# Kernel tuning notes

Hardware: AMD Instinct MI355X
Metric: run time of the kernel (lower is better)

## Reference

```python
import jax, jax.numpy as jnp
import numpy as np

EMBED_DIM = 1024
NUM_HEAD = 16
HEAD_DIM = EMBED_DIM // NUM_HEAD


def _linear_params(key, in_dim, out_dim):
    kw, kb = jax.random.split(key)
    bound = 1.0 / np.sqrt(in_dim)
    W = jax.random.uniform(kw, (out_dim, in_dim), minval=-bound, maxval=bound, dtype=jnp.float32)
    b = jax.random.uniform(kb, (out_dim,), minval=-bound, maxval=bound, dtype=jnp.float32)
    return W, b


def setup_inputs() -> dict:
    key = jax.random.key(0)
    ks = jax.random.split(key, 7)
    N, S, E = 2, 2048, EMBED_DIM
    k = jax.random.normal(ks[0], (N, S, E), dtype=jnp.float32)
    q = jax.random.normal(ks[1], (N, S, E), dtype=jnp.float32)
    v = jax.random.normal(ks[2], (N, S, E), dtype=jnp.float32)
    Wk, bk = _linear_params(ks[3], E, E)
    Wq, bq = _linear_params(ks[4], E, E)
    Wv, bv = _linear_params(ks[5], E, E)
    Wo, bo = _linear_params(ks[6], E, E)
    return {"key": k, "query": q, "value": v,
            "Wk": Wk, "bk": bk, "Wq": Wq, "bq": bq,
            "Wv": Wv, "bv": bv, "Wo": Wo, "bo": bo}


def reference(key, query, value, Wk, bk, Wq, bq, Wv, bv, Wo, bo):
    N, S_in, E = key.shape
    S_out = query.shape[1]
    H, D = NUM_HEAD, HEAD_DIM
    # projections (torch Linear: x @ W.T + b), split heads -> [N, H, S, D]
    k = (key @ Wk.T + bk).reshape(N, S_in, H, D).transpose(0, 2, 1, 3)
    q = (query @ Wq.T + bq).reshape(N, S_out, H, D).transpose(0, 2, 1, 3)
    v = (value @ Wv.T + bv).reshape(N, S_in, H, D).transpose(0, 2, 1, 3)
    # unfused attention: full [N,H,S_out,S_in] score matrix, scale, softmax
    weight = jnp.einsum("nhqd,nhkd->nhqk", q, k) / jnp.sqrt(jnp.float32(D))
    weight = jax.nn.softmax(weight, axis=-1)
    attn = jnp.einsum("nhqk,nhkd->nhqd", weight, v)  # [N,H,S_out,D]
    attn = attn.transpose(0, 2, 1, 3).reshape(N, S_out, E)
    return attn @ Wo.T + bo
```

## Files before the change

### kernel.cpp

```cpp
#include <hip/hip_runtime.h>

constexpr int E  = 1024;
constexpr int NH = 16;
constexpr int HD = 64;
constexpr int S  = 2048;
constexpr int NB = 2;
constexpr int M  = NB * S;

typedef unsigned short u16;
typedef _Float16 f16;
typedef __attribute__((ext_vector_type(8))) _Float16 h8v;
typedef __attribute__((ext_vector_type(2))) __fp16 hp2v;
typedef __attribute__((ext_vector_type(4))) float f4v;

__device__ __forceinline__ f4v mfmaH(h8v a, h8v b, f4v c) {
    return __builtin_amdgcn_mfma_f32_16x16x32_f16(a, b, c, 0, 0, 0);
}
__device__ __forceinline__ u16 f16bits(float x) {
    union { f16 h; u16 u; } t; t.h = (f16)x; return t.u;
}
__device__ __forceinline__ unsigned pkrtz(float a, float b) {
    union { hp2v h; unsigned u; } t;
    t.h = __builtin_amdgcn_cvt_pkrtz(a, b);
    return t.u;
}
__device__ __forceinline__ float fexp2(float x) {
    float r;
    asm("v_exp_f32 %0, %1" : "=v"(r) : "v"(x));
    return r;
}
typedef const __attribute__((address_space(1))) void gvoid;
typedef __attribute__((address_space(3))) void lvoid;
__device__ __forceinline__ void load_lds16(const u16* g, u16* l) {
    __builtin_amdgcn_global_load_lds((gvoid*)g, (lvoid*)l, 16, 0, 0);
}

__global__ __launch_bounds__(256)
void cvt_f16(const float* __restrict__ q, const float* __restrict__ k,
             const float* __restrict__ v,
             const float* __restrict__ wq, const float* __restrict__ wk,
             const float* __restrict__ wv, const float* __restrict__ wo,
             u16* __restrict__ out)
{
    const size_t ME = (size_t)M * E, EE = (size_t)E * E;
    const int z = blockIdx.y;
    const float* src = (z == 0) ? q : (z == 1) ? k : (z == 2) ? v
                     : (z == 3) ? wq : (z == 4) ? wk : (z == 5) ? wv : wo;
    const size_t len = (z < 3) ? ME : EE;
    u16* dst = out + ((z < 3) ? (size_t)z * ME : 3 * ME + (size_t)(z - 3) * EE);
    for (size_t i = ((size_t)blockIdx.x * 256 + threadIdx.x) * 8; i < len;
         i += (size_t)gridDim.x * 256 * 8) {
        float4 a = *reinterpret_cast<const float4*>(src + i);
        float4 b = *reinterpret_cast<const float4*>(src + i + 4);
        h8v o;
        o[0] = (f16)a.x; o[1] = (f16)a.y; o[2] = (f16)a.z; o[3] = (f16)a.w;
        o[4] = (f16)b.x; o[5] = (f16)b.y; o[6] = (f16)b.z; o[7] = (f16)b.w;
        *reinterpret_cast<h8v*>(dst + i) = o;
    }
}

__device__ __forceinline__ void gemm16_core(const u16* __restrict__ A,
                                            const u16* __restrict__ W,
                                            int bm, int bn, u16* lds, f4v acc[4][4])
{
    const int tid  = threadIdx.x;
    const int lane = tid & 63;
    const int wid  = tid >> 6;
    const int g = lane >> 4, c = lane & 15;
    const int wr = wid >> 1, wc = wid & 1;
    const int lrow = lane >> 3;
    const int lslot = lane & 7;
    const int sslot = lslot ^ lrow;

    for (int k0 = 0; k0 < E; k0 += 64) {
        #pragma unroll
        for (int i = 0; i < 4; ++i) {
            int rbase = wid * 32 + i * 8;
            load_lds16(A + (size_t)(bm + rbase + lrow) * E + k0 + (sslot << 3),
                       &lds[rbase * 64]);
            load_lds16(W + (size_t)(bn + rbase + lrow) * E + k0 + (sslot << 3),
                       &lds[8192 + rbase * 64]);
        }
        __syncthreads();

        h8v a[4][2];
        #pragma unroll
        for (int mf = 0; mf < 4; ++mf) {
            int row = wr * 64 + mf * 16 + c;
            #pragma unroll
            for (int ks = 0; ks < 2; ++ks)
                a[mf][ks] = *reinterpret_cast<h8v*>(
                    &lds[row * 64 + ((((ks << 2) | g) ^ (c & 7)) << 3)]);
        }
        #pragma unroll
        for (int nf = 0; nf < 4; ++nf) {
            int row = wc * 64 + nf * 16 + c;
            #pragma unroll
            for (int ks = 0; ks < 2; ++ks) {
                h8v b = *reinterpret_cast<h8v*>(
                    &lds[8192 + row * 64 + ((((ks << 2) | g) ^ (c & 7)) << 3)]);
                #pragma unroll
                for (int mf = 0; mf < 4; ++mf)
                    acc[mf][nf] = mfmaH(a[mf][ks], b, acc[mf][nf]);
            }
        }
        __syncthreads();
    }
}

__global__ __launch_bounds__(256, 3)
void qkv_gemm(const u16* __restrict__ qf, const u16* __restrict__ kf,
              const u16* __restrict__ vf,
              const u16* __restrict__ wqf, const u16* __restrict__ wkf,
              const u16* __restrict__ wvf,
              const float* __restrict__ bq, const float* __restrict__ bk,
              const float* __restrict__ bv,
              u16* __restrict__ Qattn, u16* __restrict__ KV, float scaleQ)
{
    __shared__ __align__(16) u16 lds[16384];
    const int z = blockIdx.z;
    const u16* A = (z == 0) ? qf : (z == 1) ? kf : vf;
    const u16* W = (z == 0) ? wqf : (z == 1) ? wkf : wvf;
    const float* bias = (z == 0) ? bq : (z == 1) ? bk : bv;
    const float scl = (z == 0) ? scaleQ : 1.0f;
    const int bm = blockIdx.x * 128, bn = blockIdx.y * 128;

    f4v acc[4][4];
    #pragma unroll
    for (int a = 0; a < 4; ++a)
        #pragma unroll
        for (int b = 0; b < 4; ++b) acc[a][b] = (f4v){0.f, 0.f, 0.f, 0.f};

    gemm16_core(A, W, bm, bn, lds, acc);

    const int lane = threadIdx.x & 63;
    const int g = lane >> 4, c = lane & 15;
    const int wid = threadIdx.x >> 6;
    const int wr = wid >> 1, wc = wid & 1;
    float bcol[4];
    #pragma unroll
    for (int nf = 0; nf < 4; ++nf) bcol[nf] = bias[bn + wc * 64 + nf * 16 + c];

    #pragma unroll
    for (int mf = 0; mf < 4; ++mf)
        #pragma unroll
        for (int r = 0; r < 4; ++r) {
            int m  = bm + wr * 64 + mf * 16 + g * 4 + r;
            int nb = m >> 11, sp = m & (S - 1);
            #pragma unroll
            for (int nf = 0; nf < 4; ++nf) {
                int ncol = bn + wc * 64 + nf * 16 + c;
                int h = ncol >> 6, d = ncol & 63;
                int bh_ = nb * NH + h;
                u16 hb = f16bits((acc[mf][nf][r] + bcol[nf]) * scl);
                if (z == 0) {
                    Qattn[((size_t)bh_ * S + sp) * HD + d] = hb;
                } else if (z == 1) {
                    int t = sp >> 6, kk = (sp >> 4) & 3, cc = sp & 15;
                    int ds = d >> 5, gg = (d >> 3) & 3, j = d & 7;
                    KV[((size_t)bh_ * 32 + t) * 8192 +
                       ((size_t)((kk * 2 + ds) * 64 + gg * 16 + cc)) * 8 + j] = hb;
                } else {
                    int t = sp >> 6, rem = sp & 63;
                    int s2 = rem >> 5, bb = (rem >> 4) & 1, gg = (rem >> 2) & 3, a2 = rem & 3;
                    int j = 4 * bb + a2;
                    int df = d >> 4, cc = d & 15;
                    KV[((size_t)bh_ * 32 + t) * 8192 + 4096 +
                       ((size_t)((df * 2 + s2) * 64 + gg * 16 + cc)) * 8 + j] = hb;
                }
            }
        }
}

__global__ __launch_bounds__(256, 3)
void out_gemm(const u16* __restrict__ A, const u16* __restrict__ W,
              const float* __restrict__ bias, float* __restrict__ C)
{
    __shared__ __align__(16) u16 lds[16384];
    const int bm = blockIdx.x * 128, bn = blockIdx.y * 128;
    f4v acc[4][4];
    #pragma unroll
    for (int a = 0; a < 4; ++a)
        #pragma unroll
        for (int b = 0; b < 4; ++b) acc[a][b] = (f4v){0.f, 0.f, 0.f, 0.f};

    gemm16_core(A, W, bm, bn, lds, acc);

    const int lane = threadIdx.x & 63;
    const int g = lane >> 4, c = lane & 15;
    const int wid = threadIdx.x >> 6;
    const int wr = wid >> 1, wc = wid & 1;
    float bcol[4];
    #pragma unroll
    for (int nf = 0; nf < 4; ++nf) bcol[nf] = bias[bn + wc * 64 + nf * 16 + c];

    #pragma unroll
    for (int mf = 0; mf < 4; ++mf)
        #pragma unroll
        for (int r = 0; r < 4; ++r) {
            int m = bm + wr * 64 + mf * 16 + g * 4 + r;
            float* crow = &C[(size_t)m * E + bn + wc * 64];
            #pragma unroll
            for (int nf = 0; nf < 4; ++nf)
                crow[nf * 16 + c] = acc[mf][nf][r] + bcol[nf];
        }
}

__global__ __launch_bounds__(128, 2)
void attn_mfma(const u16* __restrict__ Qf, const u16* __restrict__ KV,
               u16* __restrict__ Out)
{
    __shared__ __align__(16) u16 lds[8192];
    const int tid  = threadIdx.x;
    const int lane = tid & 63;
    const int wid  = tid >> 6;
    const int g = lane >> 4, c = lane & 15;
    const int dlin = blockIdx.x;
    const int idx  = dlin >> 3;
    const int bh = (dlin & 7) * 4 + (idx >> 5);
    const int qc = idx & 31;
    const int n = bh >> 4, h = bh & 15;
    const int q0 = qc * 64 + wid * 32;
    const u16* kvb = KV + (size_t)bh * 32 * 8192;
    const f4v zero4 = {0.f, 0.f, 0.f, 0.f};

    h8v Qb[2][2];
    #pragma unroll
    for (int qf = 0; qf < 2; ++qf)
        #pragma unroll
        for (int ds = 0; ds < 2; ++ds)
            Qb[qf][ds] = *reinterpret_cast<const h8v*>(
                &Qf[((size_t)bh * S + q0 + qf * 16 + c) * HD + ds * 32 + g * 8]);

    h8v ones;
    #pragma unroll
    for (int i = 0; i < 8; ++i) ones[i] = (f16)1.0f;

    f4v oacc[2][4];
    #pragma unroll
    for (int qf = 0; qf < 2; ++qf)
        #pragma unroll
        for (int df = 0; df < 4; ++df) oacc[qf][df] = zero4;
    f4v lacc[2] = {zero4, zero4};

    f4v scA[2][4], scB[2][4];
    h8v vrA[4][2], vrB[4][2];

    #define STAGE_K(T, BUFOFF)                                                  \
    {                                                                           \
        const u16* src = kvb + (size_t)(T) * 8192 + wid * 2048 + lane * 8;      \
        u16* dst = &lds[(BUFOFF) + wid * 2048];                                 \
        _Pragma("unroll")                                                       \
        for (int i = 0; i < 4; ++i) load_lds16(src + i * 512, dst + i * 512);   \
    }
    #define VLOAD(T, VR)                                                        \
    {                                                                           \
        _Pragma("unroll")                                                       \
        for (int df = 0; df < 4; ++df)                                          \
            _Pragma("unroll")                                                   \
            for (int s2 = 0; s2 < 2; ++s2)                                      \
                VR[df][s2] = *reinterpret_cast<const h8v*>(                     \
                    &kvb[(size_t)(T) * 8192 + 4096 +                            \
                         ((size_t)((df * 2 + s2) * 64 + lane)) * 8]);           \
    }

    VLOAD(0, vrA);
    STAGE_K(0, 0);
    STAGE_K(1, 4096);

    asm volatile("s_waitcnt vmcnt(4)" ::: "memory");
    __builtin_amdgcn_s_barrier();
    {
        const u16* Bt = &lds[0];
        #pragma unroll
        for (int qf = 0; qf < 2; ++qf)
            #pragma unroll
            for (int kf = 0; kf < 4; ++kf) scA[qf][kf] = zero4;
        __builtin_amdgcn_s_setprio(1);
        #pragma unroll
        for (int kf = 0; kf < 4; ++kf)
            #pragma unroll
            for (int ds = 0; ds < 2; ++ds) {
                h8v kh = *reinterpret_cast<const h8v*>(
                    &Bt[((size_t)((kf * 2 + ds) * 64 + lane)) * 8]);
                #pragma unroll
                for (int qf = 0; qf < 2; ++qf)
                    scA[qf][kf] = mfmaH(kh, Qb[qf][ds], scA[qf][kf]);
            }
        __builtin_amdgcn_s_setprio(0);
        VLOAD(1, vrB);
    }
    __builtin_amdgcn_s_barrier();
    STAGE_K(2, 0);

    #define PHASE(T, BUFOFF, SCP, SCC, VOLD, WAITN)                             \
    asm volatile("s_waitcnt vmcnt(" WAITN ")" ::: "memory");                    \
    __builtin_amdgcn_s_barrier();                                               \
    {                                                                           \
        const u16* Bt = &lds[BUFOFF];                                           \
        _Pragma("unroll")                                                       \
        for (int qf = 0; qf < 2; ++qf)                                          \
            _Pragma("unroll")                                                   \
            for (int kf = 0; kf < 4; ++kf) SCC[qf][kf] = zero4;                 \
        __builtin_amdgcn_s_setprio(1);                                          \
        _Pragma("unroll")                                                       \
        for (int kf = 0; kf < 4; ++kf)                                          \
            _Pragma("unroll")                                                   \
            for (int ds = 0; ds < 2; ++ds) {                                    \
                h8v kh = *reinterpret_cast<const h8v*>(                         \
                    &Bt[((size_t)((kf * 2 + ds) * 64 + lane)) * 8]);            \
                _Pragma("unroll")                                               \
                for (int qf = 0; qf < 2; ++qf)                                  \
                    SCC[qf][kf] = mfmaH(kh, Qb[qf][ds], SCC[qf][kf]);           \
            }                                                                   \
        __builtin_amdgcn_s_setprio(0);                                          \
        h8v pah[2][2];                                                          \
        _Pragma("unroll")                                                       \
        for (int qf = 0; qf < 2; ++qf)                                          \
            _Pragma("unroll")                                                   \
            for (int s2 = 0; s2 < 2; ++s2) {                                    \
                union { h8v v; unsigned u[4]; } th;                             \
                _Pragma("unroll")                                               \
                for (int kfh = 0; kfh < 2; ++kfh) {                             \
                    int kf = 2 * s2 + kfh;                                      \
                    float p0 = fexp2(SCP[qf][kf][0]);                           \
                    float p1 = fexp2(SCP[qf][kf][1]);                           \
                    float p2 = fexp2(SCP[qf][kf][2]);                           \
                    float p3 = fexp2(SCP[qf][kf][3]);                           \
                    th.u[2 * kfh + 0] = pkrtz(p0, p1);                          \
                    th.u[2 * kfh + 1] = pkrtz(p2, p3);                          \
                }                                                               \
                pah[qf][s2] = th.v;                                             \
            }                                                                   \
        __builtin_amdgcn_s_setprio(1);                                          \
        _Pragma("unroll")                                                       \
        for (int qf = 0; qf < 2; ++qf) {                                        \
            lacc[qf] = mfmaH(pah[qf][0], ones, lacc[qf]);                       \
            lacc[qf] = mfmaH(pah[qf][1], ones, lacc[qf]);                       \
        }                                                                       \
        _Pragma("unroll")                                                       \
        for (int df = 0; df < 4; ++df)                                          \
            _Pragma("unroll")                                                   \
            for (int s2 = 0; s2 < 2; ++s2)                                      \
                _Pragma("unroll")                                               \
                for (int qf = 0; qf < 2; ++qf)                                  \
                    oacc[qf][df] = mfmaH(pah[qf][s2], VOLD[df][s2],             \
                                         oacc[qf][df]);                         \
        __builtin_amdgcn_s_setprio(0);                                          \
        if ((T) + 1 < 32) VLOAD((T) + 1, VOLD);                                 \
    }                                                                           \
    __builtin_amdgcn_s_barrier();                                               \
    if ((T) + 2 < 32) STAGE_K((T) + 2, BUFOFF)

    for (int t = 1; t < 31; t += 2) {
        PHASE(t,     4096, scA, scB, vrA, "12");
        PHASE(t + 1, 0,    scB, scA, vrB, "12");
    }
    PHASE(31, 4096, scA, scB, vrA, "8");
    #undef PHASE
    #undef STAGE_K
    #undef VLOAD

    {
        h8v pah[2][2];
        #pragma unroll
        for (int qf = 0; qf < 2; ++qf)
            #pragma unroll
            for (int s2 = 0; s2 < 2; ++s2) {
                union { h8v v; unsigned u[4]; } th;
                #pragma unroll
                for (int kfh = 0; kfh < 2; ++kfh) {
                    int kf = 2 * s2 + kfh;
                    float p0 = fexp2(scB[qf][kf][0]);
                    float p1 = fexp2(scB[qf][kf][1]);
                    float p2 = fexp2(scB[qf][kf][2]);
                    float p3 = fexp2(scB[qf][kf][3]);
                    th.u[2 * kfh + 0] = pkrtz(p0, p1);
                    th.u[2 * kfh + 1] = pkrtz(p2, p3);
                }
                pah[qf][s2] = th.v;
            }
        #pragma unroll
        for (int qf = 0; qf < 2; ++qf) {
            lacc[qf] = mfmaH(pah[qf][0], ones, lacc[qf]);
            lacc[qf] = mfmaH(pah[qf][1], ones, lacc[qf]);
        }
        #pragma unroll
        for (int df = 0; df < 4; ++df)
            #pragma unroll
            for (int s2 = 0; s2 < 2; ++s2)
                #pragma unroll
                for (int qf = 0; qf < 2; ++qf)
                    oacc[qf][df] = mfmaH(pah[qf][s2], vrB[df][s2], oacc[qf][df]);
    }

    #pragma unroll
    for (int qf = 0; qf < 2; ++qf)
        #pragma unroll
        for (int r = 0; r < 4; ++r) {
            float linv = 1.0f / lacc[qf][r];
            int q = q0 + qf * 16 + g * 4 + r;
            size_t ob = ((size_t)n * S + q) * E + h * HD;
            #pragma unroll
            for (int df = 0; df < 4; ++df)
                Out[ob + df * 16 + c] = f16bits(oacc[qf][df][r] * linv);
        }
}

extern "C" void kernel_launch(void* const* d_in, const int* in_sizes, int n_in,
                              void* d_out, int out_size, void* d_ws, size_t ws_size,
                              hipStream_t stream)
{
    const float* key   = (const float*)d_in[0];
    const float* query = (const float*)d_in[1];
    const float* value = (const float*)d_in[2];
    const float* Wk    = (const float*)d_in[3];
    const float* bk    = (const float*)d_in[4];
    const float* Wq    = (const float*)d_in[5];
    const float* bq    = (const float*)d_in[6];
    const float* Wv    = (const float*)d_in[7];
    const float* bv    = (const float*)d_in[8];
    const float* Wo    = (const float*)d_in[9];
    const float* bo    = (const float*)d_in[10];

    const size_t ME = (size_t)M * E, EE = (size_t)E * E;
    u16* ws16  = (u16*)d_ws;
    u16* qf16  = ws16;
    u16* kf16  = ws16 + ME;
    u16* vf16  = ws16 + 2 * ME;
    u16* wqf   = ws16 + 3 * ME;
    u16* wkf   = wqf + EE;
    u16* wvf   = wkf + EE;
    u16* wof   = wvf + EE;
    u16* Qattn = wof + EE;
    u16* KV    = Qattn + ME;
    u16* AoutH = ws16;

    const float SCALE_Q = 0.125f * 1.44269504088896340736f;

    cvt_f16<<<dim3(2048, 7), 256, 0, stream>>>(query, key, value, Wq, Wk, Wv, Wo, ws16);
    qkv_gemm<<<dim3(M / 128, E / 128, 3), 256, 0, stream>>>(
        qf16, kf16, vf16, wqf, wkf, wvf, bq, bk, bv, Qattn, KV, SCALE_Q);
    attn_mfma<<<dim3((S / 64) * NB * NH), 128, 0, stream>>>(Qattn, KV, AoutH);
    out_gemm<<<dim3(M / 128, E / 128), 256, 0, stream>>>(AoutH, wof, bo, (float*)d_out);
}
```

Before: 116.0 us.

## Split attention KV range in two halves with separate combine kernel

Each attention block now handles only half of the key/value tiles, doubling the grid, and writes unnormalized fp16 partial outputs plus row sums to workspace. A new combine kernel adds the two partials, normalizes, and writes the head-interleaved output for the final GEMM. The occupancy hint is raised to 4 blocks per SM. The goal is more parallelism and better latency hiding, at the cost of an extra launch, extra memory traffic, and a shorter pipeline per block. No max subtraction is used, so the two halves can be summed directly, as in the original kernel.

Result: slower. 272.4 us (+134.9%).

```diff
diff --git a/kernel.cpp b/kernel.cpp
--- a/kernel.cpp
+++ b/kernel.cpp
@@ -206,9 +206,9 @@
         }
 }
 
-__global__ __launch_bounds__(128, 2)
+__global__ __launch_bounds__(128, 4)
 void attn_mfma(const u16* __restrict__ Qf, const u16* __restrict__ KV,
-               u16* __restrict__ Out)
+               u16* __restrict__ Opart, float* __restrict__ Lpart)
 {
     __shared__ __align__(16) u16 lds[8192];
     const int tid  = threadIdx.x;
@@ -216,11 +216,14 @@
     const int wid  = tid >> 6;
     const int g = lane >> 4, c = lane & 15;
     const int dlin = blockIdx.x;
+    const int xcd  = dlin & 7;
     const int idx  = dlin >> 3;
-    const int bh = (dlin & 7) * 4 + (idx >> 5);
-    const int qc = idx & 31;
-    const int n = bh >> 4, h = bh & 15;
+    const int bh   = xcd * 4 + (idx >> 6);
+    const int sub  = idx & 63;
+    const int qc   = sub >> 1;
+    const int half = sub & 1;
     const int q0 = qc * 64 + wid * 32;
+    const int tbase = half * 16;
     const u16* kvb = KV + (size_t)bh * 32 * 8192;
     const f4v zero4 = {0.f, 0.f, 0.f, 0.f};
 
@@ -264,9 +267,9 @@
                          ((size_t)((df * 2 + s2) * 64 + lane)) * 8]);           \
     }
 
-    VLOAD(0, vrA);
-    STAGE_K(0, 0);
-    STAGE_K(1, 4096);
+    VLOAD(tbase, vrA);
+    STAGE_K(tbase, 0);
+    STAGE_K(tbase + 1, 4096);
 
     asm volatile("s_waitcnt vmcnt(4)" ::: "memory");
     __builtin_amdgcn_s_barrier();
@@ -288,11 +291,12 @@
                     scA[qf][kf] = mfmaH(kh, Qb[qf][ds], scA[qf][kf]);
             }
         __builtin_amdgcn_s_setprio(0);
-        VLOAD(1, vrB);
+        VLOAD(tbase + 1, vrB);
     }
     __builtin_amdgcn_s_barrier();
-    STAGE_K(2, 0);
-
+    STAGE_K(tbase + 2, 0);
+
+    const int tend = tbase + 16;
     #define PHASE(T, BUFOFF, SCP, SCC, VOLD, WAITN)                             \
     asm volatile("s_waitcnt vmcnt(" WAITN ")" ::: "memory");                    \
     __builtin_amdgcn_s_barrier();                                               \
@@ -347,16 +351,16 @@
                     oacc[qf][df] = mfmaH(pah[qf][s2], VOLD[df][s2],             \
                                          oacc[qf][df]);                         \
         __builtin_amdgcn_s_setprio(0);                                          \
-        if ((T) + 1 < 32) VLOAD((T) + 1, VOLD);                                 \
+        if ((T) + 1 < tend) VLOAD((T) + 1, VOLD);                               \
     }                                                                           \
     __builtin_amdgcn_s_barrier();                                               \
-    if ((T) + 2 < 32) STAGE_K((T) + 2, BUFOFF)
-
-    for (int t = 1; t < 31; t += 2) {
+    if ((T) + 2 < tend) STAGE_K((T) + 2, BUFOFF)
+
+    for (int t = tbase + 1; t < tbase + 15; t += 2) {
         PHASE(t,     4096, scA, scB, vrA, "12");
         PHASE(t + 1, 0,    scB, scA, vrB, "12");
     }
-    PHASE(31, 4096, scA, scB, vrA, "8");
+    PHASE(tbase + 15, 4096, scA, scB, vrA, "8");
     #undef PHASE
     #undef STAGE_K
     #undef VLOAD
@@ -394,17 +398,39 @@
                     oacc[qf][df] = mfmaH(pah[qf][s2], vrB[df][s2], oacc[qf][df]);
     }
 
+    const size_t obase = (size_t)(half * 32 + bh) * S;
     #pragma unroll
     for (int qf = 0; qf < 2; ++qf)
         #pragma unroll
         for (int r = 0; r < 4; ++r) {
-            float linv = 1.0f / lacc[qf][r];
             int q = q0 + qf * 16 + g * 4 + r;
-            size_t ob = ((size_t)n * S + q) * E + h * HD;
+            size_t ob = (obase + q) * HD;
             #pragma unroll
             for (int df = 0; df < 4; ++df)
-                Out[ob + df * 16 + c] = f16bits(oacc[qf][df][r] * linv);
-        }
+                Opart[ob + df * 16 + c] = f16bits(oacc[qf][df][r]);
+            if (c == 0) Lpart[obase + q] = lacc[qf][r];
+        }
+}
+
+__global__ __launch_bounds__(256)
+void combine(const u16* __restrict__ Opart, const float* __restrict__ Lpart,
+             u16* __restrict__ AoutH)
+{
+    const size_t HSTRIDE = (size_t)32 * S * HD;
+    size_t idx8 = (size_t)blockIdx.x * 256 + threadIdx.x;
+    int row = (int)(idx8 >> 3);
+    int bh = row >> 11, q = row & (S - 1);
+    int d0 = ((int)idx8 & 7) * 8;
+    size_t o0 = (size_t)row * HD + d0;
+    h8v a = *reinterpret_cast<const h8v*>(Opart + o0);
+    h8v b = *reinterpret_cast<const h8v*>(Opart + o0 + HSTRIDE);
+    float linv = 1.0f / (Lpart[row] + Lpart[(size_t)32 * S + row]);
+    h8v o;
+    #pragma unroll
+    for (int i = 0; i < 8; ++i)
+        o[i] = (f16)(((float)a[i] + (float)b[i]) * linv);
+    int n = bh >> 4, h = bh & 15;
+    *reinterpret_cast<h8v*>(&AoutH[((size_t)n * S + q) * E + h * HD + d0]) = o;
 }
 
 extern "C" void kernel_launch(void* const* d_in, const int* in_sizes, int n_in,
@@ -434,13 +460,16 @@
     u16* wof   = wvf + EE;
     u16* Qattn = wof + EE;
     u16* KV    = Qattn + ME;
-    u16* AoutH = ws16;
+    float* Lpart = (float*)(KV + 2 * ME);
+    u16* Opart = kf16;
+    u16* AoutH = qf16;
 
     const float SCALE_Q = 0.125f * 1.44269504088896340736f;
 
     cvt_f16<<<dim3(2048, 7), 256, 0, stream>>>(query, key, value, Wq, Wk, Wv, Wo, ws16);
     qkv_gemm<<<dim3(M / 128, E / 128, 3), 256, 0, stream>>>(
         qf16, kf16, vf16, wqf, wkf, wvf, bq, bk, bv, Qattn, KV, SCALE_Q);
-    attn_mfma<<<dim3((S / 64) * NB * NH), 128, 0, stream>>>(Qattn, KV, AoutH);
+    attn_mfma<<<dim3((S / 64) * NB * NH * 2), 128, 0, stream>>>(Qattn, KV, Opart, Lpart);
+    combine<<<dim3(ME / 8 / 256), 256, 0, stream>>>(Opart, Lpart, AoutH);
     out_gemm<<<dim3(M / 128, E / 128), 256, 0, stream>>>(AoutH, wof, bo, (float*)d_out);
 }
```
